# Kernel tuning notes

Measured on AMD Instinct MI355X. Metric: run time of the kernel, lower is better.

## Reference

```python
import jax, jax.numpy as jnp
import numpy as np
import math

B, S, D, H = 1, 2048, 2048, 16
DH = D // H  # 128
HALF = DH // 2  # 64


def setup_inputs() -> dict:
    key = jax.random.key(0)
    ks = jax.random.split(key, 6)
    x = jax.random.normal(ks[0], (B, S, D), dtype=jnp.float32)
    # rotary frequencies: freqs_cis = exp(i * t * theta), theta_j = 10000^{-2j/DH}
    inv_freq = 1.0 / (10000.0 ** (np.arange(0, DH, 2, dtype=np.float32) / DH))  # [HALF]
    t = np.arange(S, dtype=np.float32)
    angles = np.outer(t, inv_freq)  # [S, HALF]
    freqs_cos = jnp.asarray(np.cos(angles), dtype=jnp.float32)
    freqs_sin = jnp.asarray(np.sin(angles), dtype=jnp.float32)
    # additive causal mask [1,1,S,S]
    mask = jnp.triu(jnp.full((S, S), -1e9, dtype=jnp.float32), k=1)[None, None]
    scale = 0.02
    wq = jax.random.normal(ks[1], (D, D), dtype=jnp.float32) * scale
    wk = jax.random.normal(ks[2], (D, D), dtype=jnp.float32) * scale
    wv = jax.random.normal(ks[3], (D, D), dtype=jnp.float32) * scale
    wo = jax.random.normal(ks[4], (D, D), dtype=jnp.float32) * scale
    return {"x": x, "freqs_cos": freqs_cos, "freqs_sin": freqs_sin, "mask": mask,
            "wq": wq, "wk": wk, "wv": wv, "wo": wo, "start_pos": 0}


def _apply_rope(t, cos, sin):
    # t: [B,S,H,DH]; cos/sin: [S,HALF] broadcast as [1,S,1,HALF]
    tr = t.reshape(*t.shape[:-1], HALF, 2)
    even, odd = tr[..., 0], tr[..., 1]
    c = cos[None, :, None, :]
    s = sin[None, :, None, :]
    out_even = even * c - odd * s
    out_odd = even * s + odd * c
    return jnp.stack([out_even, out_odd], axis=-1).reshape(t.shape)


def reference(x, freqs_cos, freqs_sin, mask, wq, wk, wv, wo, start_pos):
    bsz, seqlen, _ = x.shape
    q = (x @ wq.T).reshape(bsz, seqlen, H, DH)
    k = (x @ wk.T).reshape(bsz, seqlen, H, DH)
    v = (x @ wv.T).reshape(bsz, seqlen, H, DH)
    q = _apply_rope(q, freqs_cos, freqs_sin)
    k = _apply_rope(k, freqs_cos, freqs_sin)
    q = q.transpose(0, 2, 1, 3)  # [B,H,S,DH]
    k = k.transpose(0, 2, 1, 3)
    v = v.transpose(0, 2, 1, 3)
    scores = jnp.einsum('bhqd,bhkd->bhqk', q, k) / math.sqrt(DH) + mask
    probs = jax.nn.softmax(scores, axis=-1)
    out = jnp.einsum('bhqk,bhkd->bhqd', probs, v)  # [B,H,S,DH]
    # faithful to original: transpose(2,3) then view(bsz, seqlen, dim)
    out = out.transpose(0, 1, 3, 2).reshape(bsz, seqlen, D)
    return out @ wo.T
```

## Files before the change

kernel.cpp:

```cpp
#include <hip/hip_runtime.h>

typedef unsigned short u16;
typedef unsigned int   u32;
typedef short  short8   __attribute__((ext_vector_type(8)));
typedef float  floatx4  __attribute__((ext_vector_type(4)));
typedef u16    ushortx2 __attribute__((ext_vector_type(2)));
typedef u16    ushortx4 __attribute__((ext_vector_type(4)));

__device__ __forceinline__ float bf2f(u16 u) {
  union { u32 i; float f; } v; v.i = ((u32)u) << 16; return v.f;
}
__device__ __forceinline__ u16 f2bf(float x) {
  union { float f; u32 i; } v; v.f = x;
  u32 r = v.i + 0x7FFFu + ((v.i >> 16) & 1u);
  return (u16)(r >> 16);
}

#define GLOAD_LDS16(gptr, lptr)                                                   \
  __builtin_amdgcn_global_load_lds(                                               \
      (const __attribute__((address_space(1))) void*)(gptr),                      \
      (__attribute__((address_space(3))) void*)(lptr), 16, 0, 0)

__global__ __launch_bounds__(256) void cvt_bf16(const floatx4* __restrict__ in,
                                                ushortx4* __restrict__ out) {
  int i = blockIdx.x * 256 + threadIdx.x;
  floatx4 v = in[i];
  ushortx4 o;
  o.x = f2bf(v.x); o.y = f2bf(v.y); o.z = f2bf(v.z); o.w = f2bf(v.w);
  out[i] = o;
}

__global__ __launch_bounds__(256) void cvt_bf16_w4(
    const floatx4* __restrict__ a, const floatx4* __restrict__ b,
    const floatx4* __restrict__ c, const floatx4* __restrict__ d,
    ushortx4* __restrict__ oa, ushortx4* __restrict__ ob,
    ushortx4* __restrict__ oc, ushortx4* __restrict__ od) {
  int i = blockIdx.x * 256 + threadIdx.x;
  const floatx4* in; ushortx4* out;
  switch (blockIdx.y) {
    case 0:  in = a; out = oa; break;
    case 1:  in = b; out = ob; break;
    case 2:  in = c; out = oc; break;
    default: in = d; out = od; break;
  }
  floatx4 v = in[i];
  ushortx4 o;
  o.x = f2bf(v.x); o.y = f2bf(v.y); o.z = f2bf(v.z); o.w = f2bf(v.w);
  out[i] = o;
}

__global__ __launch_bounds__(256) void gemm_bt(
    const u16* __restrict__ A, const u16* __restrict__ B, void* __restrict__ Cv,
    int M, int N, int K, int lda, int ldb, int ldc,
    long batchA, long batchB, long batchC, int outBF16) {
  const int m0 = blockIdx.y << 7;
  const int n0 = blockIdx.x << 7;

  A += (long)blockIdx.z * batchA;
  B += (long)blockIdx.z * batchB;
  const long cbase = (long)blockIdx.z * batchC;

  __shared__ __align__(16) u16 As[128][32];
  __shared__ __align__(16) u16 Bs[128][32];

  const int t = threadIdx.x;
  const int lane = t & 63;
  const int wave = t >> 6;
  const int wm = (wave >> 1) << 6;
  const int wn = (wave & 1) << 6;
  const int quad = lane >> 4;
  const int mrow = lane & 15;

  floatx4 acc[4][4] = {};

  const int srow = (wave << 5) + (lane >> 2);
  const int sseg = (((lane & 3) ^ ((lane >> 3) & 3)) << 3);
  const u16* gA = A + (long)(m0 + srow) * lda + sseg;
  const u16* gB = B + (long)(n0 + srow) * ldb + sseg;
  u16* ldsA0 = &As[(wave << 5)][0];
  u16* ldsA1 = &As[(wave << 5) + 16][0];
  u16* ldsB0 = &Bs[(wave << 5)][0];
  u16* ldsB1 = &Bs[(wave << 5) + 16][0];

  const int qsw = ((quad ^ ((mrow >> 1) & 3)) << 3);

  for (int k0 = 0; k0 < K; k0 += 32) {
    __syncthreads();
    GLOAD_LDS16(gA + k0,            ldsA0);
    GLOAD_LDS16(gA + k0 + 16 * lda, ldsA1);
    GLOAD_LDS16(gB + k0,            ldsB0);
    GLOAD_LDS16(gB + k0 + 16 * ldb, ldsB1);
    __syncthreads();

    short8 af[4], bfr[4];
#pragma unroll
    for (int i = 0; i < 4; i++)
      af[i] = *(const short8*)&As[wm + (i << 4) + mrow][qsw];
#pragma unroll
    for (int j = 0; j < 4; j++)
      bfr[j] = *(const short8*)&Bs[wn + (j << 4) + mrow][qsw];
#pragma unroll
    for (int i = 0; i < 4; i++)
#pragma unroll
      for (int j = 0; j < 4; j++)
        acc[i][j] = __builtin_amdgcn_mfma_f32_16x16x32_bf16(af[i], bfr[j], acc[i][j], 0, 0, 0);
  }

#pragma unroll
  for (int i = 0; i < 4; i++) {
    int row0 = m0 + wm + (i << 4) + (quad << 2);
#pragma unroll
    for (int j = 0; j < 4; j++) {
      int col = n0 + wn + (j << 4) + mrow;
#pragma unroll
      for (int r = 0; r < 4; r++) {
        long idx = cbase + (long)(row0 + r) * ldc + col;
        float val = acc[i][j][r];
        if (outBF16) ((u16*)Cv)[idx] = f2bf(val);
        else         ((float*)Cv)[idx] = val;
      }
    }
  }
}

__global__ __launch_bounds__(256) void transpose_v(const u16* __restrict__ src,
                                                   u16* __restrict__ dst) {
  __shared__ u16 tile[64][68];
  const int d0 = blockIdx.x << 6;
  const int s0 = blockIdx.y << 6;
  const int tx = (threadIdx.x & 15) << 2;
  const int ty = threadIdx.x >> 4;
#pragma unroll
  for (int rr = 0; rr < 64; rr += 16) {
    ushortx4 v = *(const ushortx4*)(src + (size_t)(s0 + ty + rr) * 6144 + d0 + tx);
    *(ushortx4*)&tile[ty + rr][tx] = v;
  }
  __syncthreads();
#pragma unroll
  for (int rr = 0; rr < 64; rr += 16) {
    int r = ty + rr;
    ushortx4 o;
    o.x = tile[tx + 0][r]; o.y = tile[tx + 1][r];
    o.z = tile[tx + 2][r]; o.w = tile[tx + 3][r];
    *(ushortx4*)(dst + (size_t)(d0 + r) * 2048 + s0 + tx) = o;
  }
}

__global__ __launch_bounds__(256) void rope_qk(u16* __restrict__ qkv,
                                               const float* __restrict__ cs,
                                               const float* __restrict__ sn) {
  int idx = blockIdx.x * 256 + threadIdx.x;
  int p = idx & 63;
  int h = (idx >> 6) & 15;
  int s = idx >> 10;
  float c  = cs[(s << 6) | p];
  float si = sn[(s << 6) | p];
  float scale = blockIdx.y ? 1.0f : 0.08838834764831845f;
  size_t off = (size_t)s * 6144 + (blockIdx.y ? 2048 : 0) + (h << 7) + (p << 1);
  ushortx2 eo = *(ushortx2*)(qkv + off);
  float e = bf2f(eo.x), o = bf2f(eo.y);
  ushortx2 r;
  r.x = f2bf((e * c - o * si) * scale);
  r.y = f2bf((e * si + o * c) * scale);
  *(ushortx2*)(qkv + off) = r;
}

__global__ __launch_bounds__(256, 2) void flash_attn(
    const u16* __restrict__ QKVp, const u16* __restrict__ VTp,
    u16* __restrict__ ATp) {
  const int h = blockIdx.y;
  const int u = ((int)blockIdx.x + 2 * h) & 31;
  const int qsub = (u < 16) ? (2 * u + 1) : (62 - 2 * u);
  const int q0 = qsub << 6;
  const int ktmax = qsub >> 1;

  __shared__ __align__(16) u16 KPs[128][128];
  __shared__ __align__(16) u16 Vs[128][128];

  const int t = threadIdx.x;
  const int lane = t & 63;
  const int wave = t >> 6;
  const int quad = lane >> 4;
  const int mrow = lane & 15;
  const int sw   = mrow & 7;
  const int wmS = (wave & 1) << 5;
  const int wnS = (wave >> 1) << 6;
  const int wmV = (wave >> 1) << 6;
  const int wnP = (wave & 1) << 5;

  const int r4  = lane >> 4;
  const int seg = lane & 15;
  const int c0 = ((seg ^ r4) << 3);
  const int c4 = ((seg ^ (r4 + 4)) << 3);

  const u16* qbase = QKVp + (size_t)q0 * 6144 + (h << 7);
  const u16* kbase = QKVp + 2048 + (h << 7);
  const u16* vbase = VTp + (size_t)(h << 7) * 2048;

  short8 aq[2][4];
#pragma unroll
  for (int i = 0; i < 2; i++)
#pragma unroll
    for (int kk = 0; kk < 4; kk++)
      aq[i][kk] = *(const short8*)(qbase + (size_t)(wmS + (i << 4) + mrow) * 6144 +
                                   (kk << 5) + (quad << 3));

  const short8 ones = {0x3F80, 0x3F80, 0x3F80, 0x3F80,
                       0x3F80, 0x3F80, 0x3F80, 0x3F80};

  floatx4 Oa[4][2] = {};
  floatx4 Oa1[2] = {};

  for (int kt = 0; kt <= ktmax; kt++) {
    __syncthreads();
    {
      int r0 = wave << 5;
#pragma unroll
      for (int ii = 0; ii < 8; ii++) {
        int rr = r0 + (ii << 2);
        GLOAD_LDS16(kbase + (size_t)((kt << 7) + rr + r4) * 6144 + ((ii & 1) ? c4 : c0),
                    &KPs[rr][0]);
        GLOAD_LDS16(vbase + (size_t)(rr + r4) * 2048 + (kt << 7) + ((ii & 1) ? c4 : c0),
                    &Vs[rr][0]);
      }
    }
    __syncthreads();

    floatx4 sa[2][4] = {};
#pragma unroll
    for (int kk = 0; kk < 4; kk++) {
      short8 bk[4];
#pragma unroll
      for (int j = 0; j < 4; j++)
        bk[j] = *(const short8*)&KPs[wnS + (j << 4) + mrow][(((kk << 2) | quad) ^ sw) << 3];
#pragma unroll
      for (int i = 0; i < 2; i++)
#pragma unroll
        for (int j = 0; j < 4; j++)
          sa[i][j] = __builtin_amdgcn_mfma_f32_16x16x32_bf16(aq[i][kk], bk[j], sa[i][j], 0, 0, 0);
    }
    if (kt == ktmax) {
#pragma unroll
      for (int i = 0; i < 2; i++)
#pragma unroll
        for (int j = 0; j < 4; j++)
#pragma unroll
          for (int r = 0; r < 4; r++) {
            int ql = q0 + wmS + (i << 4) + (quad << 2) + r;
            int sl = (kt << 7) + wnS + (j << 4) + mrow;
            if (sl > ql) sa[i][j][r] = -1e30f;
          }
    }
#pragma unroll
    for (int i = 0; i < 2; i++)
#pragma unroll
      for (int j = 0; j < 4; j++)
#pragma unroll
        for (int r = 0; r < 4; r++)
          sa[i][j][r] = __expf(sa[i][j][r] - 16.f);

    __syncthreads();
#pragma unroll
    for (int i = 0; i < 2; i++)
#pragma unroll
      for (int j = 0; j < 4; j++)
#pragma unroll
        for (int r = 0; r < 4; r++) {
          int row = wmS + (i << 4) + (quad << 2) + r;
          int col = wnS + (j << 4) + mrow;
          KPs[row][((((col >> 3) ^ (row & 7)) << 3) | (col & 7))] = f2bf(sa[i][j][r]);
        }
    __syncthreads();

#pragma unroll
    for (int kk = 0; kk < 4; kk++) {
      short8 av[4], bp[2];
#pragma unroll
      for (int i = 0; i < 4; i++)
        av[i] = *(const short8*)&Vs[wmV + (i << 4) + mrow][(((kk << 2) | quad) ^ sw) << 3];
#pragma unroll
      for (int j = 0; j < 2; j++)
        bp[j] = *(const short8*)&KPs[wnP + (j << 4) + mrow][(((kk << 2) | quad) ^ sw) << 3];
#pragma unroll
      for (int i = 0; i < 4; i++)
#pragma unroll
        for (int j = 0; j < 2; j++)
          Oa[i][j] = __builtin_amdgcn_mfma_f32_16x16x32_bf16(av[i], bp[j], Oa[i][j], 0, 0, 0);
#pragma unroll
      for (int j = 0; j < 2; j++)
        Oa1[j] = __builtin_amdgcn_mfma_f32_16x16x32_bf16(ones, bp[j], Oa1[j], 0, 0, 0);
    }
  }

  float linv[2];
#pragma unroll
  for (int j = 0; j < 2; j++) linv[j] = 1.f / Oa1[j][0];
#pragma unroll
  for (int i = 0; i < 4; i++) {
    int drow = (h << 7) + wmV + (i << 4) + (quad << 2);
#pragma unroll
    for (int j = 0; j < 2; j++) {
      int col = q0 + wnP + (j << 4) + mrow;
#pragma unroll
      for (int r = 0; r < 4; r++)
        ATp[(size_t)(drow + r) * 2048 + col] = f2bf(Oa[i][j][r] * linv[j]);
    }
  }
}

__global__ __launch_bounds__(256) void reduce2(const floatx4* __restrict__ a,
                                               const floatx4* __restrict__ b,
                                               floatx4* __restrict__ o) {
  int i = blockIdx.x * 256 + threadIdx.x;
  o[i] = a[i] + b[i];
}

extern "C" void kernel_launch(void* const* d_in, const int* in_sizes, int n_in,
                              void* d_out, int out_size, void* d_ws, size_t ws_size,
                              hipStream_t stream) {
  const float* x  = (const float*)d_in[0];
  const float* fc = (const float*)d_in[1];
  const float* fs = (const float*)d_in[2];
  const float* wq = (const float*)d_in[4];
  const float* wk = (const float*)d_in[5];
  const float* wv = (const float*)d_in[6];
  const float* wo = (const float*)d_in[7];
  float* out = (float*)d_out;

  char* ws = (char*)d_ws;
  const size_t MB = 1024 * 1024;
  u16*   XB   = (u16*)(ws + 0 * MB);
  u16*   WQKV = (u16*)(ws + 8 * MB);
  u16*   WOb  = (u16*)(ws + 32 * MB);
  u16*   QKV  = (u16*)(ws + 40 * MB);
  u16*   VT   = (u16*)(ws + 64 * MB);
  u16*   AT   = (u16*)(ws + 72 * MB);
  float* PART = (float*)(ws + 80 * MB);

  int use_split = (ws_size >= 113 * MB);

  dim3 blk(256);
  cvt_bf16<<<4096, blk, 0, stream>>>((const floatx4*)x, (ushortx4*)XB);
  cvt_bf16_w4<<<dim3(4096, 4), blk, 0, stream>>>(
      (const floatx4*)wq, (const floatx4*)wk, (const floatx4*)wv, (const floatx4*)wo,
      (ushortx4*)WQKV, (ushortx4*)(WQKV + (size_t)2048 * 2048),
      (ushortx4*)(WQKV + (size_t)4096 * 2048), (ushortx4*)WOb);

  gemm_bt<<<dim3(48, 16, 1), blk, 0, stream>>>(XB, WQKV, QKV, 2048, 6144, 2048,
                                               2048, 2048, 6144, 0, 0, 0, 1);

  transpose_v<<<dim3(32, 32), blk, 0, stream>>>(QKV + 4096, VT);
  rope_qk<<<dim3(8192, 2), blk, 0, stream>>>(QKV, fc, fs);

  flash_attn<<<dim3(32, 16), blk, 0, stream>>>(QKV, VT, AT);

  if (use_split) {
    gemm_bt<<<dim3(16, 16, 2), blk, 0, stream>>>(AT, WOb, PART, 2048, 2048, 1024,
                                                 2048, 2048, 2048,
                                                 1024, 1024, (long)2048 * 2048, 0);
    reduce2<<<4096, blk, 0, stream>>>((const floatx4*)PART,
                                      (const floatx4*)(PART + (size_t)2048 * 2048),
                                      (floatx4*)out);
  } else {
    gemm_bt<<<dim3(16, 16, 1), blk, 0, stream>>>(AT, WOb, out, 2048, 2048, 2048,
                                                 2048, 2048, 2048, 0, 0, 0, 0);
  }
}
```

Baseline: 314.4 us.

## Widen GEMM K-tile, split P buffer, use exp2, reorder attention blocks

Five separate changes. The two bf16 conversion kernels are merged into one launch. The GEMM K step goes from 32 to 64 with a new 8-way XOR swizzle, so the loop runs half as many iterations and barrier pairs. Flash attention gets its own LDS buffer for P, which removes one barrier per tile, and it uses exp2 with log2e folded into the Q scale and the offset constant. Attention blocks are now ordered heaviest causal rows first to balance work across CUs. The costs are more LDS use (which may reduce occupancy) and a slight change in rounding from the folded scale.

```diff
diff --git a/kernel.cpp b/kernel.cpp
--- a/kernel.cpp
+++ b/kernel.cpp
@@ -16,32 +16,31 @@
   return (u16)(r >> 16);
 }
 
+#if __has_builtin(__builtin_amdgcn_exp2f)
+#define EXP2F(x) __builtin_amdgcn_exp2f(x)
+#else
+#define EXP2F(x) __exp2f(x)
+#endif
+
 #define GLOAD_LDS16(gptr, lptr)                                                   \
   __builtin_amdgcn_global_load_lds(                                               \
       (const __attribute__((address_space(1))) void*)(gptr),                      \
       (__attribute__((address_space(3))) void*)(lptr), 16, 0, 0)
 
-__global__ __launch_bounds__(256) void cvt_bf16(const floatx4* __restrict__ in,
-                                                ushortx4* __restrict__ out) {
-  int i = blockIdx.x * 256 + threadIdx.x;
-  floatx4 v = in[i];
-  ushortx4 o;
-  o.x = f2bf(v.x); o.y = f2bf(v.y); o.z = f2bf(v.z); o.w = f2bf(v.w);
-  out[i] = o;
-}
-
-__global__ __launch_bounds__(256) void cvt_bf16_w4(
-    const floatx4* __restrict__ a, const floatx4* __restrict__ b,
-    const floatx4* __restrict__ c, const floatx4* __restrict__ d,
-    ushortx4* __restrict__ oa, ushortx4* __restrict__ ob,
-    ushortx4* __restrict__ oc, ushortx4* __restrict__ od) {
+__global__ __launch_bounds__(256) void cvt_all(
+    const floatx4* __restrict__ x,  const floatx4* __restrict__ wq,
+    const floatx4* __restrict__ wk, const floatx4* __restrict__ wv,
+    const floatx4* __restrict__ wo,
+    ushortx4* __restrict__ xb, ushortx4* __restrict__ wqkv,
+    ushortx4* __restrict__ wob) {
   int i = blockIdx.x * 256 + threadIdx.x;
   const floatx4* in; ushortx4* out;
   switch (blockIdx.y) {
-    case 0:  in = a; out = oa; break;
-    case 1:  in = b; out = ob; break;
-    case 2:  in = c; out = oc; break;
-    default: in = d; out = od; break;
+    case 0:  in = x;  out = xb; break;
+    case 1:  in = wq; out = wqkv; break;
+    case 2:  in = wk; out = wqkv + (size_t)1048576; break;
+    case 3:  in = wv; out = wqkv + (size_t)2097152; break;
+    default: in = wo; out = wob; break;
   }
   floatx4 v = in[i];
   ushortx4 o;
@@ -60,8 +59,8 @@
   B += (long)blockIdx.z * batchB;
   const long cbase = (long)blockIdx.z * batchC;
 
-  __shared__ __align__(16) u16 As[128][32];
-  __shared__ __align__(16) u16 Bs[128][32];
+  __shared__ __align__(16) u16 As[128][64];
+  __shared__ __align__(16) u16 Bs[128][64];
 
   const int t = threadIdx.x;
   const int lane = t & 63;
@@ -70,40 +69,40 @@
   const int wn = (wave & 1) << 6;
   const int quad = lane >> 4;
   const int mrow = lane & 15;
+  const int sw8 = mrow & 7;
 
   floatx4 acc[4][4] = {};
 
-  const int srow = (wave << 5) + (lane >> 2);
-  const int sseg = (((lane & 3) ^ ((lane >> 3) & 3)) << 3);
-  const u16* gA = A + (long)(m0 + srow) * lda + sseg;
-  const u16* gB = B + (long)(n0 + srow) * ldb + sseg;
-  u16* ldsA0 = &As[(wave << 5)][0];
-  u16* ldsA1 = &As[(wave << 5) + 16][0];
-  u16* ldsB0 = &Bs[(wave << 5)][0];
-  u16* ldsB1 = &Bs[(wave << 5) + 16][0];
-
-  const int qsw = ((quad ^ ((mrow >> 1) & 3)) << 3);
-
-  for (int k0 = 0; k0 < K; k0 += 32) {
-    __syncthreads();
-    GLOAD_LDS16(gA + k0,            ldsA0);
-    GLOAD_LDS16(gA + k0 + 16 * lda, ldsA1);
-    GLOAD_LDS16(gB + k0,            ldsB0);
-    GLOAD_LDS16(gB + k0 + 16 * ldb, ldsB1);
-    __syncthreads();
-
-    short8 af[4], bfr[4];
-#pragma unroll
-    for (int i = 0; i < 4; i++)
-      af[i] = *(const short8*)&As[wm + (i << 4) + mrow][qsw];
-#pragma unroll
-    for (int j = 0; j < 4; j++)
-      bfr[j] = *(const short8*)&Bs[wn + (j << 4) + mrow][qsw];
-#pragma unroll
-    for (int i = 0; i < 4; i++)
+  const int srow = lane >> 3;
+  const int gseg = (((lane & 7) ^ srow) << 3);
+  const u16* gA = A + (long)(m0 + (wave << 5) + srow) * lda + gseg;
+  const u16* gB = B + (long)(n0 + (wave << 5) + srow) * ldb + gseg;
+
+  for (int k0 = 0; k0 < K; k0 += 64) {
+    __syncthreads();
+#pragma unroll
+    for (int ii = 0; ii < 4; ii++) {
+      GLOAD_LDS16(gA + k0 + (size_t)(ii << 3) * lda, &As[(wave << 5) + (ii << 3)][0]);
+      GLOAD_LDS16(gB + k0 + (size_t)(ii << 3) * ldb, &Bs[(wave << 5) + (ii << 3)][0]);
+    }
+    __syncthreads();
+
+#pragma unroll
+    for (int kh = 0; kh < 2; kh++) {
+      const int sidx = ((kh << 2) | quad) ^ sw8;
+      short8 af[4], bfr[4];
+#pragma unroll
+      for (int i = 0; i < 4; i++)
+        af[i] = *(const short8*)&As[wm + (i << 4) + mrow][sidx << 3];
 #pragma unroll
       for (int j = 0; j < 4; j++)
-        acc[i][j] = __builtin_amdgcn_mfma_f32_16x16x32_bf16(af[i], bfr[j], acc[i][j], 0, 0, 0);
+        bfr[j] = *(const short8*)&Bs[wn + (j << 4) + mrow][sidx << 3];
+#pragma unroll
+      for (int i = 0; i < 4; i++)
+#pragma unroll
+        for (int j = 0; j < 4; j++)
+          acc[i][j] = __builtin_amdgcn_mfma_f32_16x16x32_bf16(af[i], bfr[j], acc[i][j], 0, 0, 0);
+    }
   }
 
 #pragma unroll
@@ -155,7 +154,7 @@
   int s = idx >> 10;
   float c  = cs[(s << 6) | p];
   float si = sn[(s << 6) | p];
-  float scale = blockIdx.y ? 1.0f : 0.08838834764831845f;
+  float scale = blockIdx.y ? 1.0f : 0.12751743f;
   size_t off = (size_t)s * 6144 + (blockIdx.y ? 2048 : 0) + (h << 7) + (p << 1);
   ushortx2 eo = *(ushortx2*)(qkv + off);
   float e = bf2f(eo.x), o = bf2f(eo.y);
@@ -168,14 +167,15 @@
 __global__ __launch_bounds__(256, 2) void flash_attn(
     const u16* __restrict__ QKVp, const u16* __restrict__ VTp,
     u16* __restrict__ ATp) {
-  const int h = blockIdx.y;
-  const int u = ((int)blockIdx.x + 2 * h) & 31;
-  const int qsub = (u < 16) ? (2 * u + 1) : (62 - 2 * u);
+  const int r0id = (int)blockIdx.x + ((int)blockIdx.y << 5);
+  const int h    = r0id & 15;
+  const int qsub = 31 - (r0id >> 4);
   const int q0 = qsub << 6;
   const int ktmax = qsub >> 1;
 
-  __shared__ __align__(16) u16 KPs[128][128];
+  __shared__ __align__(16) u16 Ks[128][128];
   __shared__ __align__(16) u16 Vs[128][128];
+  __shared__ __align__(16) u16 Ps[64][128];
 
   const int t = threadIdx.x;
   const int lane = t & 63;
@@ -211,15 +211,17 @@
   floatx4 Oa[4][2] = {};
   floatx4 Oa1[2] = {};
 
+  const float C2 = 23.083120654223414f;
+
   for (int kt = 0; kt <= ktmax; kt++) {
     __syncthreads();
     {
-      int r0 = wave << 5;
+      int rr0 = wave << 5;
 #pragma unroll
       for (int ii = 0; ii < 8; ii++) {
-        int rr = r0 + (ii << 2);
+        int rr = rr0 + (ii << 2);
         GLOAD_LDS16(kbase + (size_t)((kt << 7) + rr + r4) * 6144 + ((ii & 1) ? c4 : c0),
-                    &KPs[rr][0]);
+                    &Ks[rr][0]);
         GLOAD_LDS16(vbase + (size_t)(rr + r4) * 2048 + (kt << 7) + ((ii & 1) ? c4 : c0),
                     &Vs[rr][0]);
       }
@@ -232,7 +234,7 @@
       short8 bk[4];
 #pragma unroll
       for (int j = 0; j < 4; j++)
-        bk[j] = *(const short8*)&KPs[wnS + (j << 4) + mrow][(((kk << 2) | quad) ^ sw) << 3];
+        bk[j] = *(const short8*)&Ks[wnS + (j << 4) + mrow][(((kk << 2) | quad) ^ sw) << 3];
 #pragma unroll
       for (int i = 0; i < 2; i++)
 #pragma unroll
@@ -256,19 +258,11 @@
 #pragma unroll
       for (int j = 0; j < 4; j++)
 #pragma unroll
-        for (int r = 0; r < 4; r++)
-          sa[i][j][r] = __expf(sa[i][j][r] - 16.f);
-
-    __syncthreads();
-#pragma unroll
-    for (int i = 0; i < 2; i++)
-#pragma unroll
-      for (int j = 0; j < 4; j++)
-#pragma unroll
         for (int r = 0; r < 4; r++) {
           int row = wmS + (i << 4) + (quad << 2) + r;
           int col = wnS + (j << 4) + mrow;
-          KPs[row][((((col >> 3) ^ (row & 7)) << 3) | (col & 7))] = f2bf(sa[i][j][r]);
+          Ps[row][((((col >> 3) ^ (row & 7)) << 3) | (col & 7))] =
+              f2bf(EXP2F(sa[i][j][r] - C2));
         }
     __syncthreads();
 
@@ -280,7 +274,7 @@
         av[i] = *(const short8*)&Vs[wmV + (i << 4) + mrow][(((kk << 2) | quad) ^ sw) << 3];
 #pragma unroll
       for (int j = 0; j < 2; j++)
-        bp[j] = *(const short8*)&KPs[wnP + (j << 4) + mrow][(((kk << 2) | quad) ^ sw) << 3];
+        bp[j] = *(const short8*)&Ps[wnP + (j << 4) + mrow][(((kk << 2) | quad) ^ sw) << 3];
 #pragma unroll
       for (int i = 0; i < 4; i++)
 #pragma unroll
@@ -340,11 +334,10 @@
   int use_split = (ws_size >= 113 * MB);
 
   dim3 blk(256);
-  cvt_bf16<<<4096, blk, 0, stream>>>((const floatx4*)x, (ushortx4*)XB);
-  cvt_bf16_w4<<<dim3(4096, 4), blk, 0, stream>>>(
-      (const floatx4*)wq, (const floatx4*)wk, (const floatx4*)wv, (const floatx4*)wo,
-      (ushortx4*)WQKV, (ushortx4*)(WQKV + (size_t)2048 * 2048),
-      (ushortx4*)(WQKV + (size_t)4096 * 2048), (ushortx4*)WOb);
+  cvt_all<<<dim3(4096, 5), blk, 0, stream>>>(
+      (const floatx4*)x, (const floatx4*)wq, (const floatx4*)wk,
+      (const floatx4*)wv, (const floatx4*)wo,
+      (ushortx4*)XB, (ushortx4*)WQKV, (ushortx4*)WOb);
 
   gemm_bt<<<dim3(48, 16, 1), blk, 0, stream>>>(XB, WQKV, QKV, 2048, 6144, 2048,
                                                2048, 2048, 6144, 0, 0, 0, 1);
```

New measurement: 302.5 us. 1.04x faster.
